# Kernel tuning notes

Measured on AMD Instinct MI355X. Metric: run time of the kernel, lower is better.

Reference implementation:

```python
import jax, jax.numpy as jnp
import numpy as np

N = 100000   # nodes
E = 1600000  # edges (avg degree 16)
D = 64       # input feature dim


def _lin(k, i, o):
    return (jax.random.normal(k, (i, o), jnp.float32) / np.float32(np.sqrt(i)))


def setup_inputs() -> dict:
    key = jax.random.key(0)
    ks = jax.random.split(key, 12)
    return {
        "x": jax.random.normal(ks[0], (N, D), jnp.float32),
        "edge_index": jax.random.randint(ks[1], (2, E), 0, N, dtype=jnp.int64),
        # layer 1: SAGEConv(64, 64, 'pool')
        "W1_pool": _lin(ks[2], 64, 64), "b1_pool": jnp.zeros((64,), jnp.float32),
        "W1_self": _lin(ks[3], 64, 64), "W1_neigh": _lin(ks[4], 64, 64),
        "b1": jnp.zeros((64,), jnp.float32),
        # layer 2: SAGEConv(64, 32, 'pool')
        "W2_pool": _lin(ks[5], 64, 64), "b2_pool": jnp.zeros((64,), jnp.float32),
        "W2_self": _lin(ks[6], 64, 32), "W2_neigh": _lin(ks[7], 64, 32),
        "b2": jnp.zeros((32,), jnp.float32),
        # layer 3: SAGEConv(32, 32, 'mean')
        "W3_self": _lin(ks[8], 32, 32), "W3_neigh": _lin(ks[9], 32, 32),
        "b3": jnp.zeros((32,), jnp.float32),
    }


def _sage_pool(x, src, dst, Wp, bp, Ws, Wn, b):
    # max-pool aggregator: transform all nodes once (cheaper than per-edge),
    # gather per-edge, segment-max into destination nodes.
    m = jax.nn.relu(x @ Wp + bp)[src]                      # [E, in]
    agg = jax.ops.segment_max(m, dst, num_segments=N)     # [N, in]
    agg = jnp.where(jnp.isfinite(agg), agg, jnp.float32(0.0))  # isolated nodes -> 0
    return x @ Ws + agg @ Wn + b


def _sage_mean(x, src, dst, Ws, Wn, b):
    s = jax.ops.segment_sum(x[src], dst, num_segments=N)   # [N, in]
    cnt = jax.ops.segment_sum(jnp.ones((src.shape[0],), jnp.float32), dst,
                              num_segments=N)
    agg = s / jnp.maximum(cnt, jnp.float32(1.0))[:, None]
    return x @ Ws + agg @ Wn + b


def reference(x, edge_index,
              W1_pool, b1_pool, W1_self, W1_neigh, b1,
              W2_pool, b2_pool, W2_self, W2_neigh, b2,
              W3_self, W3_neigh, b3):
    src, dst = edge_index[0], edge_index[1]
    h = jax.nn.relu(_sage_pool(x, src, dst, W1_pool, b1_pool, W1_self, W1_neigh, b1))
    h = _sage_pool(h, src, dst, W2_pool, b2_pool, W2_self, W2_neigh, b2)
    h = _sage_mean(h, src, dst, W3_self, W3_neigh, b3)
    return h
```

## Files before the change

kernel.cpp:

```cpp
#include <hip/hip_runtime.h>
#include <hip/hip_bf16.h>


typedef unsigned int uint;
typedef short short8 __attribute__((ext_vector_type(8)));
typedef float f32x4 __attribute__((ext_vector_type(4)));
typedef float f32x2 __attribute__((ext_vector_type(2)));
typedef unsigned short u16x8 __attribute__((ext_vector_type(8)));

__device__ __forceinline__ float bf2f(unsigned short h){
  return __uint_as_float(((uint)h) << 16);
}
__device__ __forceinline__ unsigned short f2bf(float f){
  uint u = __float_as_uint(f);
  u += 0x7fffu + ((u >> 16) & 1u);
  return (unsigned short)(u >> 16);
}
__device__ __forceinline__ float lo16(uint u){ return __uint_as_float(u << 16); }
__device__ __forceinline__ float hi16(uint u){ return __uint_as_float(u & 0xffff0000u); }

__device__ __forceinline__ uint4 pkmax4(uint4 a, uint4 b){
  u16x8 x = __builtin_bit_cast(u16x8, a);
  u16x8 y = __builtin_bit_cast(u16x8, b);
  return __builtin_bit_cast(uint4, __builtin_elementwise_max(x, y));
}
__device__ __forceinline__ f32x2 b2lo(uint u){
  f32x2 r; r.x = lo16(u); r.y = hi16(u); return r;
}

struct WConv {
  const void* src[13];
  int n[13], isbias[13], Cs[13], K[13], off[13];
};

__global__ void conv_w(WConv wc, unsigned short* wtbase, float* bbase,
                       const unsigned short* x, const int* ei,
                       int* flags, int* ccur, int NB){
  __shared__ int sflags[2];
  int t = threadIdx.x;
  if (t < 64){
    int sane = 0;
    #pragma unroll
    for (int k = 0; k < 4; ++k){
      int e = (x[(t * 4 + k) * 2] >> 7) & 0xff;
      sane += (e >= 118 && e <= 134);
    }
    #pragma unroll
    for (int off = 32; off; off >>= 1) sane += __shfl_down(sane, off, 64);
    unsigned long long b = __ballot(ei[1 + 2 * t] != 0);
    if (t == 0){ sflags[0] = (sane >= 128); sflags[1] = (b == 0ull); }
  }
  __syncthreads();
  int isbf = sflags[0];
  if (blockIdx.x == 0){
    if (t == 0){ flags[0] = sflags[0]; flags[1] = sflags[1]; }
    for (int i = t; i < NB; i += 256) ccur[i] = 0;
  }
  int bt = blockIdx.x, n = wc.n[bt];
  if (wc.isbias[bt]){
    float* d = bbase + wc.off[bt];
    for (int i = t; i < n; i += 256)
      d[i] = isbf ? bf2f(((const unsigned short*)wc.src[bt])[i])
                  : ((const float*)wc.src[bt])[i];
  } else {
    unsigned short* d = wtbase + wc.off[bt];
    int Cs = wc.Cs[bt], K = wc.K[bt], Cm = (1 << Cs) - 1;
    for (int i = t; i < n; i += 256){
      int k = i >> Cs, c = i & Cm;
      unsigned short v = isbf ? ((const unsigned short*)wc.src[bt])[i]
                              : f2bf(((const float*)wc.src[bt])[i]);
      d[c * K + k] = v;
    }
  }
}

__device__ __forceinline__ void load_edge(const void* ei, int E, int is64, int e,
                                          int& s, int& d){
  if (is64){
    const long long* p = (const long long*)ei;
    s = (int)p[e]; d = (int)p[E + e];
  } else {
    const int* p = (const int*)ei;
    s = p[e]; d = p[E + e];
  }
}

__device__ __forceinline__ short8 ld_fragA_bf16(const unsigned short* A, int row,
                                                int K, int koff){
  return *(const short8*)(A + (size_t)row * K + koff);
}
__device__ __forceinline__ short8 ld_fragA_f32(const float* A, int row,
                                               int K, int koff){
  const float* q = A + (size_t)row * K + koff;
  float4 f0 = *(const float4*)q;
  float4 f1 = *(const float4*)(q + 4);
  short8 r;
  r[0] = (short)f2bf(f0.x); r[1] = (short)f2bf(f0.y);
  r[2] = (short)f2bf(f0.z); r[3] = (short)f2bf(f0.w);
  r[4] = (short)f2bf(f1.x); r[5] = (short)f2bf(f1.y);
  r[6] = (short)f2bf(f1.z); r[7] = (short)f2bf(f1.w);
  return r;
}
__device__ __forceinline__ unsigned short f2bf_relu(float f){
  return (unsigned short)(f2bf(fmaxf(f, 0.f)) & 0x7fff);
}

#define CSR_CE 8192

__device__ __forceinline__ void phase1_body(
    const void* __restrict__ ei, const int* __restrict__ flags,
    int* __restrict__ ccur, uint* __restrict__ pairs,
    int E, int N, int NB, int S, int CAP, int blk,
    uint* hist, uint* gbase)
{
  int t = threadIdx.x;
  uint dmask = (1u << S) - 1u;
  int is64 = flags[1];
  int e0 = blk * CSR_CE;
  for (int i = t; i < 1024; i += 256) hist[i] = 0;
  __syncthreads();
  #pragma unroll 4
  for (int it = 0; it < CSR_CE / 256; ++it){
    int e = e0 + it * 256 + t;
    if (e >= E) break;
    int s, d; load_edge(ei, E, is64, e, s, d);
    if ((unsigned)s >= (unsigned)N || (unsigned)d >= (unsigned)N) continue;
    atomicAdd(&hist[d >> S], 1u);
  }
  __syncthreads();
  for (int b = t; b < NB; b += 256){
    uint c = hist[b];
    if (c) gbase[b] = (uint)atomicAdd(&ccur[b], (int)c);
    hist[b] = 0;
  }
  __syncthreads();
  #pragma unroll 4
  for (int it = 0; it < CSR_CE / 256; ++it){
    int e = e0 + it * 256 + t;
    if (e >= E) break;
    int s, d; load_edge(ei, E, is64, e, s, d);
    if ((unsigned)s >= (unsigned)N || (unsigned)d >= (unsigned)N) continue;
    int b = d >> S;
    uint local = atomicAdd(&hist[b], 1u);
    uint pos = gbase[b] + local;
    if (pos >= (uint)CAP) pos = (uint)CAP - 1;
    pairs[(size_t)b * CAP + pos] = ((uint)s << S) | ((uint)d & dmask);
  }
}

template<int AMODE>
__device__ __forceinline__ void mm1_body(
    const void* __restrict__ Av, const unsigned short* __restrict__ WaT,
    const float* __restrict__ bias, const int* __restrict__ flags,
    unsigned short* __restrict__ out, int N, int blk)
{
  int wid = threadIdx.x >> 6, lane = threadIdx.x & 63;
  int n0 = blk * 32;
  int m = lane & 15, quad = lane >> 4, koq = quad * 8;
  int colbase = wid * 16;
  int rowc0 = min(n0 + m, N - 1);
  int rowc1 = min(n0 + 16 + m, N - 1);
  bool af32 = (AMODE == 2) && (flags[0] == 0);
  f32x4 a0 = {0.f,0.f,0.f,0.f}, a1 = {0.f,0.f,0.f,0.f};
  #pragma unroll
  for (int k0 = 0; k0 < 64; k0 += 32){
    short8 af0 = af32 ? ld_fragA_f32((const float*)Av, rowc0, 64, k0 + koq)
                      : ld_fragA_bf16((const unsigned short*)Av, rowc0, 64, k0 + koq);
    short8 af1 = af32 ? ld_fragA_f32((const float*)Av, rowc1, 64, k0 + koq)
                      : ld_fragA_bf16((const unsigned short*)Av, rowc1, 64, k0 + koq);
    short8 wf = *(const short8*)(WaT + (size_t)(colbase + m) * 64 + k0 + koq);
    a0 = __builtin_amdgcn_mfma_f32_16x16x32_bf16(af0, wf, a0, 0, 0, 0);
    a1 = __builtin_amdgcn_mfma_f32_16x16x32_bf16(af1, wf, a1, 0, 0, 0);
  }
  float bv = bias[colbase + m];
  #pragma unroll
  for (int r = 0; r < 4; ++r){
    int rl = quad * 4 + r;
    if (n0 + rl < N)
      out[(size_t)(n0 + rl) * 64 + colbase + m] = f2bf_relu(a0[r] + bv);
    if (n0 + 16 + rl < N)
      out[(size_t)(n0 + 16 + rl) * 64 + colbase + m] = f2bf_relu(a1[r] + bv);
  }
}

template<int AMODE>
__global__ __launch_bounds__(256) void phase1_mm1(
    const void* __restrict__ ei, const int* __restrict__ flags,
    int* __restrict__ ccur, uint* __restrict__ pairs,
    int E, int N, int NB, int S, int CAP, int nP,
    const void* __restrict__ x, const unsigned short* __restrict__ W1pT,
    const float* __restrict__ b1p, unsigned short* __restrict__ mbuf)
{
  __shared__ uint hist[1024];
  __shared__ uint gbase[1024];
  if ((int)blockIdx.x < nP)
    phase1_body(ei, flags, ccur, pairs, E, N, NB, S, CAP, blockIdx.x, hist, gbase);
  else
    mm1_body<AMODE>(x, W1pT, b1p, flags, mbuf, N, blockIdx.x - nP);
}

__global__ void csr_scan0(const int* __restrict__ ccur, int* __restrict__ cbase,
                          int* __restrict__ rowptrN, int NB, int CAP)
{
  __shared__ int sm[256];
  int t = threadIdx.x;
  int g = (NB + 255) / 256;
  int vb = t * g, v[4], s = 0;
  for (int k = 0; k < g; ++k){
    int i = vb + k; int x = (i < NB) ? min(ccur[i], CAP) : 0; v[k] = x; s += x;
  }
  sm[t] = s; __syncthreads();
  for (int off = 1; off < 256; off <<= 1){
    int x = (t >= off) ? sm[t - off] : 0;
    __syncthreads(); sm[t] += x; __syncthreads();
  }
  int run = sm[t] - s;
  for (int k = 0; k < g; ++k){
    int i = vb + k;
    if (i < NB){ cbase[i] = run; run += v[k]; }
  }
  if (t == 255){ cbase[NB] = run; *rowptrN = run; }
}

#define P2_CAP 6144
__global__ __launch_bounds__(256) void csr_phase2(
    const int* __restrict__ cbase, const int* __restrict__ ccur,
    const uint* __restrict__ pairs,
    int* __restrict__ bucket, int* __restrict__ row_ptr, int N, int S, int CAP)
{
  __shared__ int lbuf[P2_CAP];
  __shared__ int cur[1024];
  __shared__ int sm[256];
  int b = blockIdx.x, t = threadIdx.x;
  uint dmask = (1u << S) - 1u;
  int n0 = b << S;
  int n1 = n0 + (1 << S); if (n1 > N) n1 = N;
  int nn = n1 - n0;
  int base = cbase[b];
  int cnt = min(ccur[b], CAP);
  const uint* bp = pairs + (size_t)b * CAP;

  for (int i = t; i < nn; i += 256) cur[i] = 0;
  __syncthreads();
  for (int j = t; j < cnt; j += 256)
    atomicAdd(&cur[(int)(bp[j] & dmask)], 1);
  __syncthreads();
  int g = (nn + 255) / 256, vb = t * g, v[4], s = 0;
  for (int k = 0; k < g; ++k){
    int i = vb + k; int x = (i < nn) ? cur[i] : 0; v[k] = x; s += x;
  }
  sm[t] = s; __syncthreads();
  for (int off = 1; off < 256; off <<= 1){
    int x = (t >= off) ? sm[t - off] : 0;
    __syncthreads(); sm[t] += x; __syncthreads();
  }
  int run = sm[t] - s;
  for (int k = 0; k < g; ++k){
    int i = vb + k;
    if (i < nn){ row_ptr[n0 + i] = base + run; cur[i] = run; run += v[k]; }
  }
  __syncthreads();
  if (cnt <= 0) return;
  if (cnt <= P2_CAP){
    for (int j = t; j < cnt; j += 256){
      uint pr = bp[j];
      int pos = atomicAdd(&cur[(int)(pr & dmask)], 1);
      lbuf[pos] = (int)(pr >> S);
    }
    __syncthreads();
    for (int i = t; i < cnt; i += 256) bucket[base + i] = lbuf[i];
  } else {
    for (int j = t; j < cnt; j += 256){
      uint pr = bp[j];
      int pos = atomicAdd(&cur[(int)(pr & dmask)], 1);
      bucket[base + pos] = (int)(pr >> S);
    }
  }
}

__device__ __forceinline__ void gmax_oct8(
    const int* __restrict__ row_ptr, const int* __restrict__ bucket,
    const unsigned short* __restrict__ m,
    unsigned short* la_base, int LDH, int node0, int N, int lane)
{
  int ni = lane >> 3;
  int col = (lane & 7) * 8;
  int node = node0 + ni;
  int nc = min(node, N - 1);
  int rs = row_ptr[nc];
  int re = row_ptr[nc + 1];
  int cnt = (node < N) ? (re - rs) : 0;
  uint4 acc = {0u, 0u, 0u, 0u};
  int t = 0;
  for (; t + 4 <= cnt; t += 4){
    int s0 = bucket[rs + t];
    int s1 = bucket[rs + t + 1];
    int s2 = bucket[rs + t + 2];
    int s3 = bucket[rs + t + 3];
    uint4 v0 = *(const uint4*)(m + (size_t)s0 * 64 + col);
    uint4 v1 = *(const uint4*)(m + (size_t)s1 * 64 + col);
    uint4 v2 = *(const uint4*)(m + (size_t)s2 * 64 + col);
    uint4 v3 = *(const uint4*)(m + (size_t)s3 * 64 + col);
    acc = pkmax4(acc, pkmax4(pkmax4(v0, v1), pkmax4(v2, v3)));
  }
  for (; t < cnt; ++t){
    int s = bucket[rs + t];
    uint4 v = *(const uint4*)(m + (size_t)s * 64 + col);
    acc = pkmax4(acc, v);
  }
  *(uint4*)(la_base + (size_t)ni * LDH + col) = acc;
}

template<int AMODE>
__global__ __launch_bounds__(256) void gmax_mm_fused(
    const void* __restrict__ Av, const unsigned short* __restrict__ msrc,
    const int* __restrict__ row_ptr, const int* __restrict__ bucket,
    const unsigned short* __restrict__ WaT, const unsigned short* __restrict__ WbT,
    const float* __restrict__ bias1,
    const unsigned short* __restrict__ WcT, const float* __restrict__ bias2,
    const int* __restrict__ flags,
    unsigned short* __restrict__ out1, unsigned short* __restrict__ out2, int N)
{
  constexpr int K = 64, C = 64, LDH = 72;
  __shared__ unsigned short la[32 * LDH];
  __shared__ unsigned short hl[32 * LDH];
  int wid = threadIdx.x >> 6, lane = threadIdx.x & 63;
  int n0 = blockIdx.x * 32;
  gmax_oct8(row_ptr, bucket, msrc, la + (size_t)(wid * 8) * LDH, LDH,
            n0 + wid * 8, N, lane);
  __syncthreads();
  int m = lane & 15, quad = lane >> 4, koq = quad * 8;
  int colbase = wid * 16;
  int rowc0 = min(n0 + m, N - 1);
  int rowc1 = min(n0 + 16 + m, N - 1);
  bool af32 = (AMODE == 2) && (flags[0] == 0);

  f32x4 a0 = {0.f,0.f,0.f,0.f}, a1 = {0.f,0.f,0.f,0.f};
  #pragma unroll
  for (int k0 = 0; k0 < K; k0 += 32){
    short8 af0 = af32 ? ld_fragA_f32((const float*)Av, rowc0, K, k0 + koq)
                      : ld_fragA_bf16((const unsigned short*)Av, rowc0, K, k0 + koq);
    short8 af1 = af32 ? ld_fragA_f32((const float*)Av, rowc1, K, k0 + koq)
                      : ld_fragA_bf16((const unsigned short*)Av, rowc1, K, k0 + koq);
    short8 wf = *(const short8*)(WaT + (size_t)(colbase + m) * K + k0 + koq);
    a0 = __builtin_amdgcn_mfma_f32_16x16x32_bf16(af0, wf, a0, 0, 0, 0);
    a1 = __builtin_amdgcn_mfma_f32_16x16x32_bf16(af1, wf, a1, 0, 0, 0);
    short8 bf0 = *(const short8*)(la + m * LDH + k0 + koq);
    short8 bf1 = *(const short8*)(la + (16 + m) * LDH + k0 + koq);
    short8 wg = *(const short8*)(WbT + (size_t)(colbase + m) * K + k0 + koq);
    a0 = __builtin_amdgcn_mfma_f32_16x16x32_bf16(bf0, wg, a0, 0, 0, 0);
    a1 = __builtin_amdgcn_mfma_f32_16x16x32_bf16(bf1, wg, a1, 0, 0, 0);
  }
  float bv = bias1[colbase + m];
  #pragma unroll
  for (int r = 0; r < 4; ++r){
    int rl = quad * 4 + r;
    unsigned short h0 = f2bf_relu(a0[r] + bv);
    unsigned short h1v = f2bf_relu(a1[r] + bv);
    hl[rl * LDH + colbase + m] = h0;
    hl[(16 + rl) * LDH + colbase + m] = h1v;
    if (n0 + rl < N) out1[(size_t)(n0 + rl) * C + colbase + m] = h0;
    if (n0 + 16 + rl < N) out1[(size_t)(n0 + 16 + rl) * C + colbase + m] = h1v;
  }
  __syncthreads();
  f32x4 c0 = {0.f,0.f,0.f,0.f}, c1 = {0.f,0.f,0.f,0.f};
  #pragma unroll
  for (int k0 = 0; k0 < K; k0 += 32){
    short8 q0 = *(const short8*)(hl + m * LDH + k0 + koq);
    short8 q1 = *(const short8*)(hl + (16 + m) * LDH + k0 + koq);
    short8 wf = *(const short8*)(WcT + (size_t)(colbase + m) * K + k0 + koq);
    c0 = __builtin_amdgcn_mfma_f32_16x16x32_bf16(q0, wf, c0, 0, 0, 0);
    c1 = __builtin_amdgcn_mfma_f32_16x16x32_bf16(q1, wf, c1, 0, 0, 0);
  }
  float b2v = bias2[colbase + m];
  #pragma unroll
  for (int r = 0; r < 4; ++r){
    int rl = quad * 4 + r;
    if (n0 + rl < N)
      out2[(size_t)(n0 + rl) * C + colbase + m] = f2bf_relu(c0[r] + b2v);
    if (n0 + 16 + rl < N)
      out2[(size_t)(n0 + 16 + rl) * C + colbase + m] = f2bf_relu(c1[r] + b2v);
  }
}

__global__ __launch_bounds__(256) void gmax_mm2(
    const unsigned short* __restrict__ h1, const unsigned short* __restrict__ msrc,
    const int* __restrict__ row_ptr, const int* __restrict__ bucket,
    const unsigned short* __restrict__ WsT, const unsigned short* __restrict__ WnT,
    const float* __restrict__ bias, unsigned short* __restrict__ h2, int N)
{
  constexpr int LDH = 72;
  __shared__ unsigned short la[64 * LDH];
  int wid = threadIdx.x >> 6, lane = threadIdx.x & 63;
  int n0 = blockIdx.x * 64;
  gmax_oct8(row_ptr, bucket, msrc, la + (size_t)(wid * 16) * LDH, LDH,
            n0 + wid * 16, N, lane);
  gmax_oct8(row_ptr, bucket, msrc, la + (size_t)(wid * 16 + 8) * LDH, LDH,
            n0 + wid * 16 + 8, N, lane);
  __syncthreads();
  int m = lane & 15, quad = lane >> 4, koq = quad * 8;
  int colbase = (wid & 1) * 16;
  int rb = (wid >> 1) * 32;
  int rowc0 = min(n0 + rb + m, N - 1), rowc1 = min(n0 + rb + 16 + m, N - 1);
  f32x4 a0 = {0.f,0.f,0.f,0.f}, a1 = {0.f,0.f,0.f,0.f};
  #pragma unroll
  for (int k0 = 0; k0 < 64; k0 += 32){
    short8 af0 = *(const short8*)(h1 + (size_t)rowc0 * 64 + k0 + koq);
    short8 af1 = *(const short8*)(h1 + (size_t)rowc1 * 64 + k0 + koq);
    short8 wf = *(const short8*)(WsT + (size_t)(colbase + m) * 64 + k0 + koq);
    a0 = __builtin_amdgcn_mfma_f32_16x16x32_bf16(af0, wf, a0, 0, 0, 0);
    a1 = __builtin_amdgcn_mfma_f32_16x16x32_bf16(af1, wf, a1, 0, 0, 0);
    short8 bf0 = *(const short8*)(la + (rb + m) * LDH + k0 + koq);
    short8 bf1 = *(const short8*)(la + (rb + 16 + m) * LDH + k0 + koq);
    short8 wg = *(const short8*)(WnT + (size_t)(colbase + m) * 64 + k0 + koq);
    a0 = __builtin_amdgcn_mfma_f32_16x16x32_bf16(bf0, wg, a0, 0, 0, 0);
    a1 = __builtin_amdgcn_mfma_f32_16x16x32_bf16(bf1, wg, a1, 0, 0, 0);
  }
  float bv = bias[colbase + m];
  #pragma unroll
  for (int r = 0; r < 4; ++r){
    int rl = quad * 4 + r;
    if (n0 + rb + rl < N)
      h2[(size_t)(n0 + rb + rl) * 32 + colbase + m] = f2bf(a0[r] + bv);
    if (n0 + rb + 16 + rl < N)
      h2[(size_t)(n0 + rb + 16 + rl) * 32 + colbase + m] = f2bf(a1[r] + bv);
  }
}

__global__ __launch_bounds__(256) void gsum3(
    const int* __restrict__ row_ptr, const int* __restrict__ bucket,
    const unsigned short* __restrict__ h2,
    const unsigned short* __restrict__ W3sT, const unsigned short* __restrict__ W3nT,
    const float* __restrict__ b3, float* __restrict__ out, int N)
{
  constexpr int LDA = 40;
  __shared__ unsigned short la[16 * LDA];
  int t = threadIdx.x;
  int w = t >> 6, lane = t & 63;
  int n0 = blockIdx.x * 16;
  int g = lane >> 4, q = lane & 15;
  int nd = n0 + w * 4 + g;
  int ndc = nd < N ? nd : N - 1;
  int rs = row_ptr[ndc];
  int cnt = (nd < N) ? (row_ptr[ndc + 1] - rs) : 0;
  int fg8 = (q & 3) * 8, rowsel = q >> 2;
  f32x2 a0 = {0.f,0.f}, a1 = {0.f,0.f}, a2 = {0.f,0.f}, a3 = {0.f,0.f};
  for (int c0 = 0; c0 < cnt; c0 += 16){
    int chunk = min(cnt - c0, 16);
    int bval = (q < chunk) ? bucket[rs + c0 + q] : 0;
    int it = (chunk + 3) >> 2;
    for (int k = 0; k < it; ++k){
      int j = k * 4 + rowsel;
      int s = __shfl(bval, (g << 4) + j, 64);
      uint4 v = *(const uint4*)(h2 + (size_t)s * 32 + fg8);
      if (j < chunk){
        a0 += b2lo(v.x); a1 += b2lo(v.y); a2 += b2lo(v.z); a3 += b2lo(v.w);
      }
    }
  }
  #pragma unroll
  for (int off = 4; off <= 8; off <<= 1){
    a0.x += __shfl_xor(a0.x, off, 64); a0.y += __shfl_xor(a0.y, off, 64);
    a1.x += __shfl_xor(a1.x, off, 64); a1.y += __shfl_xor(a1.y, off, 64);
    a2.x += __shfl_xor(a2.x, off, 64); a2.y += __shfl_xor(a2.y, off, 64);
    a3.x += __shfl_xor(a3.x, off, 64); a3.y += __shfl_xor(a3.y, off, 64);
  }
  if (rowsel == 0){
    float sc = 1.f / fmaxf((float)cnt, 1.f);
    int r = w * 4 + g;
    uint4 pk;
    pk.x = (uint)f2bf(a0.x * sc) | ((uint)f2bf(a0.y * sc) << 16);
    pk.y = (uint)f2bf(a1.x * sc) | ((uint)f2bf(a1.y * sc) << 16);
    pk.z = (uint)f2bf(a2.x * sc) | ((uint)f2bf(a2.y * sc) << 16);
    pk.w = (uint)f2bf(a3.x * sc) | ((uint)f2bf(a3.y * sc) << 16);
    *(uint4*)(la + r * LDA + q * 8) = pk;
  }
  __syncthreads();
  if (w < 2){
    int m = lane & 15, quad = lane >> 4, koq = quad * 8;
    int colbase = w * 16;
    int row = n0 + m;
    int rowc = row < N ? row : N - 1;
    f32x4 acc = {0.f, 0.f, 0.f, 0.f};
    short8 aself = *(const short8*)(h2 + (size_t)rowc * 32 + koq);
    short8 wfs = *(const short8*)(W3sT + (size_t)(colbase + m) * 32 + koq);
    acc = __builtin_amdgcn_mfma_f32_16x16x32_bf16(aself, wfs, acc, 0, 0, 0);
    short8 aagg = *(const short8*)(la + m * LDA + koq);
    short8 wfn = *(const short8*)(W3nT + (size_t)(colbase + m) * 32 + koq);
    acc = __builtin_amdgcn_mfma_f32_16x16x32_bf16(aagg, wfn, acc, 0, 0, 0);
    float bv = b3[colbase + m];
    #pragma unroll
    for (int r = 0; r < 4; ++r){
      int orow = n0 + quad * 4 + r;
      if (orow < N) out[(size_t)orow * 32 + colbase + m] = acc[r] + bv;
    }
  }
}

static inline char* align256(char* p){
  return (char*)(((uintptr_t)p + 255) & ~(uintptr_t)255);
}

extern "C" void kernel_launch(void* const* d_in, const int* in_sizes, int n_in,
                              void* d_out, int out_size, void* d_ws, size_t ws_size,
                              hipStream_t stream)
{
  const void* x = d_in[0];
  const void* ei = d_in[1];
  int N = in_sizes[0] / 64;
  int E = in_sizes[1] / 2;

  char* ws = (char*)d_ws;
  unsigned short* wtbase = (unsigned short*)ws;
  float* bbase = (float*)(ws + 65536);
  int* flags = (int*)(ws + 131072 - 256);

  int S = 7, NB = (N + 127) >> 7;
  while (NB > 1024){ S++; NB = (N + (1 << S) - 1) >> S; }
  int CAP = ((2 * E / NB) + 255) & ~255;
  if (CAP < 1024) CAP = 1024;

  char* p = ws + 131072;
  int* row_ptr = (int*)p; p = align256(p + (size_t)(N + 1) * 4);
  int* cbase   = (int*)p; p = align256(p + 4352);
  int* ccur    = (int*)p; p = align256(p + 4352);
  int* bucket  = (int*)p; p = align256(p + (size_t)E * 4);
  uint* pairs  = (uint*)p; p = align256(p + (size_t)NB * CAP * 4);
  char* P = p;  p = align256(p + (size_t)N * 64 * 2);
  char* Q = p;  p = align256(p + (size_t)N * 64 * 2);
  char* R = p;  p = align256(p + (size_t)N * 64 * 2);
  unsigned short* m1 = (unsigned short*)P;
  unsigned short* h2 = (unsigned short*)P;
  unsigned short* m2 = (unsigned short*)Q;
  unsigned short* h1 = (unsigned short*)R;

  WConv wc;
  {
    const int widx[13] = {2, 3, 4, 5, 6, 7, 8, 9, 10, 11, 12, 13, 14};
    const int isb[13]  = {0, 1, 0, 0, 1, 0, 1, 0, 0, 1, 0, 0, 1};
    const int Cs[13]   = {6, 0, 6, 6, 0, 6, 0, 5, 5, 0, 5, 5, 0};
    const int Kk[13]   = {64, 0, 64, 64, 0, 64, 0, 64, 64, 0, 32, 32, 0};
    const int off[13]  = {0, 0, 4096, 8192, 64, 12288, 128, 16384, 18432, 192,
                          20480, 21504, 224};
    for (int i = 0; i < 13; ++i){
      wc.src[i] = d_in[widx[i]]; wc.n[i] = in_sizes[widx[i]];
      wc.isbias[i] = isb[i]; wc.Cs[i] = Cs[i]; wc.K[i] = Kk[i]; wc.off[i] = off[i];
    }
  }
  hipLaunchKernelGGL(conv_w, dim3(13), dim3(256), 0, stream, wc, wtbase, bbase,
                     (const unsigned short*)x, (const int*)ei, flags, ccur, NB);
  unsigned short* W1pT = wtbase + 0;     unsigned short* W1sT = wtbase + 4096;
  unsigned short* W1nT = wtbase + 8192;  unsigned short* W2pT = wtbase + 12288;
  unsigned short* W2sT = wtbase + 16384; unsigned short* W2nT = wtbase + 18432;
  unsigned short* W3sT = wtbase + 20480; unsigned short* W3nT = wtbase + 21504;
  float* b1p = bbase + 0;  float* b1 = bbase + 64; float* b2p = bbase + 128;
  float* b2 = bbase + 192; float* b3 = bbase + 224;

  int nP = (E + CSR_CE - 1) / CSR_CE;
  int RT32 = (N + 31) / 32;
  int RT16 = (N + 15) / 16;

  phase1_mm1<2><<<nP + RT32, 256, 0, stream>>>(
      ei, flags, ccur, pairs, E, N, NB, S, CAP, nP, x, W1pT, b1p, m1);
  csr_scan0<<<1, 256, 0, stream>>>(ccur, cbase, row_ptr + N, NB, CAP);
  csr_phase2<<<NB, 256, 0, stream>>>(cbase, ccur, pairs, bucket, row_ptr, N, S, CAP);

  gmax_mm_fused<2><<<RT32,256,0,stream>>>(
      x, m1, row_ptr, bucket, W1sT, W1nT, b1, W2pT, b2p, flags, h1, m2, N);

  gmax_mm2<<<(N + 63) / 64,256,0,stream>>>(
      h1, m2, row_ptr, bucket, W2sT, W2nT, b2, h2, N);

  gsum3<<<RT16,256,0,stream>>>(row_ptr, bucket, h2, W3sT, W3nT, b3,
                               (float*)d_out, N);
}
```

Baseline: 274.1 us.

## Split max-pool gathers into sliced-layout kernels separate from matmuls

The pooled message buffers are now stored in a column-sliced layout: 8 slices of 8 bf16 columns, each contiguous per node. A new gslice kernel does the neighbour max-gather one slice at a time, so the gathered working set per slice (N*16 bytes) can stay cache-resident. The matmul kernels now read the aggregated result from global memory instead of fusing the gather into LDS. This adds two kernel launches and an extra write and read of the aggregate buffer, in exchange for better cache locality on the random gathers.

```diff
diff --git a/kernel.cpp b/kernel.cpp
--- a/kernel.cpp
+++ b/kernel.cpp
@@ -152,7 +152,7 @@
 __device__ __forceinline__ void mm1_body(
     const void* __restrict__ Av, const unsigned short* __restrict__ WaT,
     const float* __restrict__ bias, const int* __restrict__ flags,
-    unsigned short* __restrict__ out, int N, int blk)
+    unsigned short* __restrict__ outsl, int N, int blk)
 {
   int wid = threadIdx.x >> 6, lane = threadIdx.x & 63;
   int n0 = blk * 32;
@@ -173,13 +173,15 @@
     a1 = __builtin_amdgcn_mfma_f32_16x16x32_bf16(af1, wf, a1, 0, 0, 0);
   }
   float bv = bias[colbase + m];
+  int cm = colbase + m;
+  size_t ob = (size_t)(cm >> 3) * N * 8 + (cm & 7);
   #pragma unroll
   for (int r = 0; r < 4; ++r){
     int rl = quad * 4 + r;
     if (n0 + rl < N)
-      out[(size_t)(n0 + rl) * 64 + colbase + m] = f2bf_relu(a0[r] + bv);
+      outsl[ob + (size_t)(n0 + rl) * 8] = f2bf_relu(a0[r] + bv);
     if (n0 + 16 + rl < N)
-      out[(size_t)(n0 + 16 + rl) * 64 + colbase + m] = f2bf_relu(a1[r] + bv);
+      outsl[ob + (size_t)(n0 + 16 + rl) * 8] = f2bf_relu(a1[r] + bv);
   }
 }
 
@@ -278,57 +280,50 @@
   }
 }
 
-__device__ __forceinline__ void gmax_oct8(
+__global__ __launch_bounds__(256) void gslice(
     const int* __restrict__ row_ptr, const int* __restrict__ bucket,
-    const unsigned short* __restrict__ m,
-    unsigned short* la_base, int LDH, int node0, int N, int lane)
-{
-  int ni = lane >> 3;
-  int col = (lane & 7) * 8;
-  int node = node0 + ni;
-  int nc = min(node, N - 1);
-  int rs = row_ptr[nc];
-  int re = row_ptr[nc + 1];
-  int cnt = (node < N) ? (re - rs) : 0;
+    const unsigned short* __restrict__ msl, unsigned short* __restrict__ aggsl,
+    int N)
+{
+  int slice = (int)(blockIdx.x & 7u);
+  int node = (int)(blockIdx.x >> 3) * 256 + threadIdx.x;
+  if (node >= N) return;
+  const unsigned short* base = msl + (size_t)slice * N * 8;
+  int rs = row_ptr[node];
+  int cnt = row_ptr[node + 1] - rs;
   uint4 acc = {0u, 0u, 0u, 0u};
-  int t = 0;
-  for (; t + 4 <= cnt; t += 4){
-    int s0 = bucket[rs + t];
-    int s1 = bucket[rs + t + 1];
-    int s2 = bucket[rs + t + 2];
-    int s3 = bucket[rs + t + 3];
-    uint4 v0 = *(const uint4*)(m + (size_t)s0 * 64 + col);
-    uint4 v1 = *(const uint4*)(m + (size_t)s1 * 64 + col);
-    uint4 v2 = *(const uint4*)(m + (size_t)s2 * 64 + col);
-    uint4 v3 = *(const uint4*)(m + (size_t)s3 * 64 + col);
+  int k = 0;
+  for (; k + 4 <= cnt; k += 4){
+    int s0 = bucket[rs + k];
+    int s1 = bucket[rs + k + 1];
+    int s2 = bucket[rs + k + 2];
+    int s3 = bucket[rs + k + 3];
+    uint4 v0 = *(const uint4*)(base + (size_t)s0 * 8);
+    uint4 v1 = *(const uint4*)(base + (size_t)s1 * 8);
+    uint4 v2 = *(const uint4*)(base + (size_t)s2 * 8);
+    uint4 v3 = *(const uint4*)(base + (size_t)s3 * 8);
     acc = pkmax4(acc, pkmax4(pkmax4(v0, v1), pkmax4(v2, v3)));
   }
-  for (; t < cnt; ++t){
-    int s = bucket[rs + t];
-    uint4 v = *(const uint4*)(m + (size_t)s * 64 + col);
-    acc = pkmax4(acc, v);
-  }
-  *(uint4*)(la_base + (size_t)ni * LDH + col) = acc;
+  for (; k < cnt; ++k){
+    int s = bucket[rs + k];
+    acc = pkmax4(acc, *(const uint4*)(base + (size_t)s * 8));
+  }
+  *(uint4*)(aggsl + (size_t)slice * N * 8 + (size_t)node * 8) = acc;
 }
 
 template<int AMODE>
-__global__ __launch_bounds__(256) void gmax_mm_fused(
-    const void* __restrict__ Av, const unsigned short* __restrict__ msrc,
-    const int* __restrict__ row_ptr, const int* __restrict__ bucket,
+__global__ __launch_bounds__(256) void mm_h1m2(
+    const void* __restrict__ Av, const unsigned short* __restrict__ aggsl,
     const unsigned short* __restrict__ WaT, const unsigned short* __restrict__ WbT,
     const float* __restrict__ bias1,
     const unsigned short* __restrict__ WcT, const float* __restrict__ bias2,
     const int* __restrict__ flags,
-    unsigned short* __restrict__ out1, unsigned short* __restrict__ out2, int N)
+    unsigned short* __restrict__ out1, unsigned short* __restrict__ out2sl, int N)
 {
   constexpr int K = 64, C = 64, LDH = 72;
-  __shared__ unsigned short la[32 * LDH];
   __shared__ unsigned short hl[32 * LDH];
   int wid = threadIdx.x >> 6, lane = threadIdx.x & 63;
   int n0 = blockIdx.x * 32;
-  gmax_oct8(row_ptr, bucket, msrc, la + (size_t)(wid * 8) * LDH, LDH,
-            n0 + wid * 8, N, lane);
-  __syncthreads();
   int m = lane & 15, quad = lane >> 4, koq = quad * 8;
   int colbase = wid * 16;
   int rowc0 = min(n0 + m, N - 1);
@@ -345,8 +340,9 @@
     short8 wf = *(const short8*)(WaT + (size_t)(colbase + m) * K + k0 + koq);
     a0 = __builtin_amdgcn_mfma_f32_16x16x32_bf16(af0, wf, a0, 0, 0, 0);
     a1 = __builtin_amdgcn_mfma_f32_16x16x32_bf16(af1, wf, a1, 0, 0, 0);
-    short8 bf0 = *(const short8*)(la + m * LDH + k0 + koq);
-    short8 bf1 = *(const short8*)(la + (16 + m) * LDH + k0 + koq);
+    const unsigned short* ab = aggsl + (size_t)((k0 >> 3) + quad) * N * 8;
+    short8 bf0 = *(const short8*)(ab + (size_t)rowc0 * 8);
+    short8 bf1 = *(const short8*)(ab + (size_t)rowc1 * 8);
     short8 wg = *(const short8*)(WbT + (size_t)(colbase + m) * K + k0 + koq);
     a0 = __builtin_amdgcn_mfma_f32_16x16x32_bf16(bf0, wg, a0, 0, 0, 0);
     a1 = __builtin_amdgcn_mfma_f32_16x16x32_bf16(bf1, wg, a1, 0, 0, 0);
@@ -373,31 +369,25 @@
     c1 = __builtin_amdgcn_mfma_f32_16x16x32_bf16(q1, wf, c1, 0, 0, 0);
   }
   float b2v = bias2[colbase + m];
+  int cm = colbase + m;
+  size_t ob = (size_t)(cm >> 3) * N * 8 + (cm & 7);
   #pragma unroll
   for (int r = 0; r < 4; ++r){
     int rl = quad * 4 + r;
     if (n0 + rl < N)
-      out2[(size_t)(n0 + rl) * C + colbase + m] = f2bf_relu(c0[r] + b2v);
+      out2sl[ob + (size_t)(n0 + rl) * 8] = f2bf_relu(c0[r] + b2v);
     if (n0 + 16 + rl < N)
-      out2[(size_t)(n0 + 16 + rl) * C + colbase + m] = f2bf_relu(c1[r] + b2v);
-  }
-}
-
-__global__ __launch_bounds__(256) void gmax_mm2(
-    const unsigned short* __restrict__ h1, const unsigned short* __restrict__ msrc,
-    const int* __restrict__ row_ptr, const int* __restrict__ bucket,
+      out2sl[ob + (size_t)(n0 + 16 + rl) * 8] = f2bf_relu(c1[r] + b2v);
+  }
+}
+
+__global__ __launch_bounds__(256) void mm_h2(
+    const unsigned short* __restrict__ h1, const unsigned short* __restrict__ aggsl,
     const unsigned short* __restrict__ WsT, const unsigned short* __restrict__ WnT,
     const float* __restrict__ bias, unsigned short* __restrict__ h2, int N)
 {
-  constexpr int LDH = 72;
-  __shared__ unsigned short la[64 * LDH];
   int wid = threadIdx.x >> 6, lane = threadIdx.x & 63;
   int n0 = blockIdx.x * 64;
-  gmax_oct8(row_ptr, bucket, msrc, la + (size_t)(wid * 16) * LDH, LDH,
-            n0 + wid * 16, N, lane);
-  gmax_oct8(row_ptr, bucket, msrc, la + (size_t)(wid * 16 + 8) * LDH, LDH,
-            n0 + wid * 16 + 8, N, lane);
-  __syncthreads();
   int m = lane & 15, quad = lane >> 4, koq = quad * 8;
   int colbase = (wid & 1) * 16;
   int rb = (wid >> 1) * 32;
@@ -410,8 +400,9 @@
     short8 wf = *(const short8*)(WsT + (size_t)(colbase + m) * 64 + k0 + koq);
     a0 = __builtin_amdgcn_mfma_f32_16x16x32_bf16(af0, wf, a0, 0, 0, 0);
     a1 = __builtin_amdgcn_mfma_f32_16x16x32_bf16(af1, wf, a1, 0, 0, 0);
-    short8 bf0 = *(const short8*)(la + (rb + m) * LDH + k0 + koq);
-    short8 bf1 = *(const short8*)(la + (rb + 16 + m) * LDH + k0 + koq);
+    const unsigned short* ab = aggsl + (size_t)((k0 >> 3) + quad) * N * 8;
+    short8 bf0 = *(const short8*)(ab + (size_t)rowc0 * 8);
+    short8 bf1 = *(const short8*)(ab + (size_t)rowc1 * 8);
     short8 wg = *(const short8*)(WnT + (size_t)(colbase + m) * 64 + k0 + koq);
     a0 = __builtin_amdgcn_mfma_f32_16x16x32_bf16(bf0, wg, a0, 0, 0, 0);
     a1 = __builtin_amdgcn_mfma_f32_16x16x32_bf16(bf1, wg, a1, 0, 0, 0);
@@ -529,10 +520,12 @@
   char* P = p;  p = align256(p + (size_t)N * 64 * 2);
   char* Q = p;  p = align256(p + (size_t)N * 64 * 2);
   char* R = p;  p = align256(p + (size_t)N * 64 * 2);
+  char* T = p;  p = align256(p + (size_t)N * 64 * 2);
   unsigned short* m1 = (unsigned short*)P;
   unsigned short* h2 = (unsigned short*)P;
   unsigned short* m2 = (unsigned short*)Q;
   unsigned short* h1 = (unsigned short*)R;
+  unsigned short* agg = (unsigned short*)T;
 
   WConv wc;
   {
@@ -559,18 +552,20 @@
   int nP = (E + CSR_CE - 1) / CSR_CE;
   int RT32 = (N + 31) / 32;
   int RT16 = (N + 15) / 16;
+  int GS = ((N + 255) / 256) * 8;
 
   phase1_mm1<2><<<nP + RT32, 256, 0, stream>>>(
       ei, flags, ccur, pairs, E, N, NB, S, CAP, nP, x, W1pT, b1p, m1);
   csr_scan0<<<1, 256, 0, stream>>>(ccur, cbase, row_ptr + N, NB, CAP);
   csr_phase2<<<NB, 256, 0, stream>>>(cbase, ccur, pairs, bucket, row_ptr, N, S, CAP);
 
-  gmax_mm_fused<2><<<RT32,256,0,stream>>>(
-      x, m1, row_ptr, bucket, W1sT, W1nT, b1, W2pT, b2p, flags, h1, m2, N);
-
-  gmax_mm2<<<(N + 63) / 64,256,0,stream>>>(
-      h1, m2, row_ptr, bucket, W2sT, W2nT, b2, h2, N);
-
-  gsum3<<<RT16,256,0,stream>>>(row_ptr, bucket, h2, W3sT, W3nT, b3,
-                               (float*)d_out, N);
-}
+  gslice<<<GS, 256, 0, stream>>>(row_ptr, bucket, m1, agg, N);
+  mm_h1m2<2><<<RT32, 256, 0, stream>>>(
+      x, agg, W1sT, W1nT, b1, W2pT, b2p, flags, h1, m2, N);
+
+  gslice<<<GS, 256, 0, stream>>>(row_ptr, bucket, m2, agg, N);
+  mm_h2<<<(N + 63) / 64, 256, 0, stream>>>(h1, agg, W2sT, W2nT, b2, h2, N);
+
+  gsum3<<<RT16, 256, 0, stream>>>(row_ptr, bucket, h2, W3sT, W3nT, b3,
+                                  (float*)d_out, N);
+}
```

Measured after the change: 363.8 us. +32.7%, slower.
